# Kernel tuning notes

Measured on AMD Instinct MI355X. Metric: run time of the kernel, lower is better.

Reference implementation:

```python
import jax, jax.numpy as jnp
import numpy as np

B, T, C = 2, 2048, 1024
H = 16
D = C // H  # head_dim = 64
SCALE = D ** -0.5


def setup_inputs() -> dict:
    key = jax.random.key(0)
    ks = jax.random.split(key, 5)
    x = jax.random.normal(ks[0], (B, T, C), dtype=jnp.float32)
    # causal mask: -inf above diagonal, 0 elsewhere (module checks mask == -inf)
    neg_inf = jnp.float32(-jnp.inf)
    causal = jnp.where(jnp.tril(jnp.ones((T, T), dtype=bool)), 0.0, neg_inf)
    mask = causal[None, None, :, :].astype(jnp.float32)  # [1,1,T,T]
    # xavier_normal for [C, C] linear weights: std = sqrt(2/(C+C))
    std = float(np.sqrt(2.0 / (C + C)))
    wq = jax.random.normal(ks[1], (C, C), dtype=jnp.float32) * std
    wk = jax.random.normal(ks[2], (C, C), dtype=jnp.float32) * std
    wv = jax.random.normal(ks[3], (C, C), dtype=jnp.float32) * std
    wo = jax.random.normal(ks[4], (C, C), dtype=jnp.float32) * std
    return {"x": x, "mask": mask, "wq": wq, "wk": wk, "wv": wv, "wo": wo}


def reference(x, mask, wq, wk, wv, wo):
    # torch nn.Linear: y = x @ W.T
    q = jnp.einsum('btc,oc->bto', x, wq).reshape(B, T, H, D).transpose(0, 2, 1, 3)
    k = jnp.einsum('btc,oc->bto', x, wk).reshape(B, T, H, D).transpose(0, 2, 1, 3)
    v = jnp.einsum('btc,oc->bto', x, wv).reshape(B, T, H, D).transpose(0, 2, 1, 3)
    scores = jnp.einsum('bhqd,bhkd->bhqk', q, k) * SCALE  # [B,H,T,T]
    scores = jnp.where(mask == -jnp.inf, -jnp.inf, scores)
    attn = jax.nn.softmax(scores, axis=-1)
    out = jnp.einsum('bhqk,bhkd->bhqd', attn, v)  # [B,H,T,D]
    out = out.transpose(0, 2, 1, 3).reshape(B, T, C)
    return jnp.einsum('btc,oc->bto', out, wo)
```

## Files before the change

### kernel.cpp

```cpp
#include <hip/hip_runtime.h>
#include <hip/hip_bf16.h>


typedef __bf16 bf16_t;
typedef __bf16 bf16x8 __attribute__((ext_vector_type(8)));
typedef __bf16 bf16x4 __attribute__((ext_vector_type(4)));
typedef __bf16 bf16x2 __attribute__((ext_vector_type(2)));
typedef float  f32x4  __attribute__((ext_vector_type(4)));
typedef unsigned u32x4 __attribute__((ext_vector_type(4)));

__device__ __forceinline__ void gload_lds16(const bf16_t* g, bf16_t* l) {
  __builtin_amdgcn_global_load_lds((__attribute__((address_space(1))) void*)g,
                                   (__attribute__((address_space(3))) void*)l, 16, 0, 0);
}

__device__ __forceinline__ unsigned pack_bf16(float a, float b) {
  bf16x2 v; v[0] = (bf16_t)a; v[1] = (bf16_t)b;
  return __builtin_bit_cast(unsigned, v);
}

__global__ __launch_bounds__(256) void cvt_f32_bf16(const float* __restrict__ in,
                                                    bf16_t* __restrict__ out, int n4) {
  int i = blockIdx.x * 256 + threadIdx.x;
  if (i >= n4) return;
  float4 v = reinterpret_cast<const float4*>(in)[i];
  bf16x4 o;
  o[0] = (bf16_t)v.x; o[1] = (bf16_t)v.y; o[2] = (bf16_t)v.z; o[3] = (bf16_t)v.w;
  reinterpret_cast<bf16x4*>(out)[i] = o;
}

__global__ __launch_bounds__(256) void cvt_w4(const float* __restrict__ i0, const float* __restrict__ i1,
                                              const float* __restrict__ i2, const float* __restrict__ i3,
                                              bf16_t* __restrict__ o0, bf16_t* __restrict__ o1,
                                              bf16_t* __restrict__ o2, bf16_t* __restrict__ o3) {
  int which = blockIdx.y;
  const float* in = (which == 0) ? i0 : (which == 1) ? i1 : (which == 2) ? i2 : i3;
  bf16_t* out     = (which == 0) ? o0 : (which == 1) ? o1 : (which == 2) ? o2 : o3;
  int i = blockIdx.x * 256 + threadIdx.x;
  float4 v = reinterpret_cast<const float4*>(in)[i];
  bf16x4 o;
  o[0] = (bf16_t)v.x; o[1] = (bf16_t)v.y; o[2] = (bf16_t)v.z; o[3] = (bf16_t)v.w;
  reinterpret_cast<bf16x4*>(out)[i] = o;
}

#define TM 128
#define TN 128
#define TK 64

__global__ __launch_bounds__(256) void gemm_bt(
    const bf16_t* __restrict__ A,
    const bf16_t* __restrict__ W0, const bf16_t* __restrict__ W1, const bf16_t* __restrict__ W2,
    bf16_t* __restrict__ O0, bf16_t* __restrict__ O1, bf16_t* __restrict__ O2,
    float* __restrict__ OF, int kind)
{
  __shared__ alignas(16) bf16_t As[TM * TK];
  __shared__ alignas(16) bf16_t Bs[TN * TK];
  const int K = 1024;
  const int t = threadIdx.x;
  const int lane = t & 63;
  const int w = t >> 6;
  const int wr = w >> 1, wc = w & 1;
  const int lo = lane & 15, hi = lane >> 4;
  const int m0 = blockIdx.x * TM, n0 = blockIdx.y * TN;

  int mode;
  const bf16_t* Bw;
  bf16_t* outb = nullptr;
  if (kind == 1) { mode = 3; Bw = W0; }
  else {
    mode = blockIdx.z;
    Bw   = (mode == 0) ? W0 : (mode == 1) ? W1 : W2;
    outb = (mode == 0) ? O0 : (mode == 1) ? O1 : O2;
  }

  f32x4 acc[4][4] = {};
  const int srow = t >> 3;
  const int sch  = t & 7;

  for (int k0 = 0; k0 < K; k0 += TK) {
#pragma unroll
    for (int r = 0; r < 4; ++r) {
      int row = r * 32 + srow;
      gload_lds16(A  + (size_t)(m0 + row) * K + k0 + sch * 8, &As[row * TK + sch * 8]);
      gload_lds16(Bw + (size_t)(n0 + row) * K + k0 + sch * 8, &Bs[row * TK + sch * 8]);
    }
    __syncthreads();
#pragma unroll
    for (int ks = 0; ks < 2; ++ks) {
      bf16x8 af[4], bfr[4];
#pragma unroll
      for (int i = 0; i < 4; ++i) {
        af[i]  = *reinterpret_cast<const bf16x8*>(&As[(wr * 64 + i * 16 + lo) * TK + ks * 32 + hi * 8]);
        bfr[i] = *reinterpret_cast<const bf16x8*>(&Bs[(wc * 64 + i * 16 + lo) * TK + ks * 32 + hi * 8]);
      }
#pragma unroll
      for (int i = 0; i < 4; ++i)
#pragma unroll
        for (int j = 0; j < 4; ++j)
          acc[i][j] = __builtin_amdgcn_mfma_f32_16x16x32_bf16(af[i], bfr[j], acc[i][j], 0, 0, 0);
    }
    __syncthreads();
  }

#pragma unroll
  for (int i = 0; i < 4; ++i)
#pragma unroll
    for (int j = 0; j < 4; ++j)
#pragma unroll
      for (int r = 0; r < 4; ++r) {
        int m = m0 + wr * 64 + i * 16 + hi * 4 + r;
        int n = n0 + wc * 64 + j * 16 + lo;
        float v = acc[i][j][r];
        if (mode == 3) {
          OF[(size_t)m * 1024 + n] = v;
        } else {
          int b = m >> 11, tq = m & 2047;
          int h = n >> 6,  d  = n & 63;
          if (mode == 0) v *= 0.18033688011f;
          size_t addr = (mode == 2)
              ? ((size_t)(b * 16 + h) * 64 + d) * 2048 + tq
              : ((size_t)(b * 16 + h) * 2048 + tq) * 64 + d;
          outb[addr] = (bf16_t)v;
        }
      }
}

#define SLAB 8832

__global__ __launch_bounds__(256) void attn_fwd(
    const bf16_t* __restrict__ Q,
    const bf16_t* __restrict__ Km,
    const bf16_t* __restrict__ Vt,
    bf16_t* __restrict__ att)
{
  __shared__ alignas(16) char smem[4 * SLAB];
  const int t = threadIdx.x, lane = t & 63, w = t >> 6;
  const int lo = lane & 15, h = lane >> 4;
  const int item = blockIdx.x;
  const int bh = item >> 5;
  const int pr = item & 31;
  const bf16_t* Qb = Q  + (size_t)bh * 2048 * 64;
  const bf16_t* Kb = Km + (size_t)bh * 2048 * 64;
  const bf16_t* Vb = Vt + (size_t)bh * 64 * 2048;
  float* accW = (float*)(smem + w * SLAB);
  float* lW   = (float*)(smem + w * SLAB + 8704);
  const int b = bh >> 4, hd = bh & 15;
  const int src1 = lo + 32 * (h & 1);
  const int src2 = src1 + 16;
  const bool hsel = (h >> 1) != 0;

  auto run_tile = [&](int q0) {
    bf16x8 qf[2][2];
#pragma unroll
    for (int qt = 0; qt < 2; ++qt)
#pragma unroll
      for (int ks = 0; ks < 2; ++ks)
        qf[qt][ks] = *reinterpret_cast<const bf16x8*>(
            &Qb[(size_t)(q0 + qt * 16 + lo) * 64 + ks * 32 + h * 8]);

    f32x4 acc[2][4] = {};
    float lp[2] = {};
    const int kend = q0 + 32;
    for (int kb = w * 64; kb < kend; kb += 256) {
      f32x4 s_t[4][2] = {};
#pragma unroll
      for (int ks = 0; ks < 2; ++ks) {
        bf16x8 kf[4];
#pragma unroll
        for (int kt = 0; kt < 4; ++kt)
          kf[kt] = *reinterpret_cast<const bf16x8*>(
              &Kb[(size_t)(kb + kt * 16 + lo) * 64 + ks * 32 + h * 8]);
#pragma unroll
        for (int kt = 0; kt < 4; ++kt)
#pragma unroll
          for (int qt = 0; qt < 2; ++qt)
            s_t[kt][qt] = __builtin_amdgcn_mfma_f32_16x16x32_bf16(kf[kt], qf[qt][ks], s_t[kt][qt], 0, 0, 0);
      }
      bf16x8 vf[2][4];
#pragma unroll
      for (int kh = 0; kh < 2; ++kh)
#pragma unroll
        for (int dt = 0; dt < 4; ++dt)
          vf[kh][dt] = *reinterpret_cast<const bf16x8*>(
              &Vb[(size_t)(dt * 16 + lo) * 2048 + kb + kh * 32 + h * 8]);
      if (kb + 63 >= q0) {
#pragma unroll
        for (int kt = 0; kt < 4; ++kt)
#pragma unroll
          for (int qt = 0; qt < 2; ++qt)
#pragma unroll
            for (int r = 0; r < 4; ++r) {
              int kg = kb + kt * 16 + h * 4 + r;
              int qg = q0 + qt * 16 + lo;
              if (kg > qg) s_t[kt][qt][r] = -__builtin_inff();
            }
      }
      unsigned uP[2][4][2];
#pragma unroll
      for (int qt = 0; qt < 2; ++qt)
#pragma unroll
        for (int kt = 0; kt < 4; ++kt) {
          float p0 = exp2f(s_t[kt][qt][0]);
          float p1 = exp2f(s_t[kt][qt][1]);
          float p2 = exp2f(s_t[kt][qt][2]);
          float p3 = exp2f(s_t[kt][qt][3]);
          lp[qt] += (p0 + p1) + (p2 + p3);
          uP[qt][kt][0] = pack_bf16(p0, p1);
          uP[qt][kt][1] = pack_bf16(p2, p3);
        }
#pragma unroll
      for (int kh = 0; kh < 2; ++kh)
#pragma unroll
        for (int qt = 0; qt < 2; ++qt) {
          unsigned a0x = __shfl((int)uP[qt][2 * kh][0], src1);
          unsigned a0y = __shfl((int)uP[qt][2 * kh + 1][0], src1);
          unsigned a1x = __shfl((int)uP[qt][2 * kh][1], src1);
          unsigned a1y = __shfl((int)uP[qt][2 * kh + 1][1], src1);
          unsigned a2x = __shfl((int)uP[qt][2 * kh][0], src2);
          unsigned a2y = __shfl((int)uP[qt][2 * kh + 1][0], src2);
          unsigned a3x = __shfl((int)uP[qt][2 * kh][1], src2);
          unsigned a3y = __shfl((int)uP[qt][2 * kh + 1][1], src2);
          u32x4 au;
          au[0] = hsel ? a0y : a0x;
          au[1] = hsel ? a1y : a1x;
          au[2] = hsel ? a2y : a2x;
          au[3] = hsel ? a3y : a3x;
          bf16x8 pa = __builtin_bit_cast(bf16x8, au);
#pragma unroll
          for (int dt = 0; dt < 4; ++dt)
            acc[qt][dt] = __builtin_amdgcn_mfma_f32_16x16x32_bf16(pa, vf[kh][dt], acc[qt][dt], 0, 0, 0);
        }
    }

    float lrow[2];
#pragma unroll
    for (int qt = 0; qt < 2; ++qt) {
      float v = lp[qt];
      v += __shfl_xor(v, 16);
      v += __shfl_xor(v, 32);
      lrow[qt] = v;
    }

#pragma unroll
    for (int qt = 0; qt < 2; ++qt) {
#pragma unroll
      for (int r = 0; r < 4; ++r) {
        int row = qt * 16 + h * 4 + r;
#pragma unroll
        for (int dt = 0; dt < 4; ++dt)
          accW[row * 68 + dt * 16 + lo] = acc[qt][dt][r];
      }
      if (h == 0) lW[qt * 16 + lo] = lrow[qt];
    }
    __syncthreads();

    {
      const int row = t >> 3, c0 = (t & 7) * 8;
      float lsum = 0.f, o[8] = {};
#pragma unroll
      for (int w2 = 0; w2 < 4; ++w2) {
        lsum += ((const float*)(smem + w2 * SLAB + 8704))[row];
        const float* a2 = (const float*)(smem + w2 * SLAB) + row * 68 + c0;
#pragma unroll
        for (int j = 0; j < 8; ++j) o[j] += a2[j];
      }
      float inv = 1.f / lsum;
      bf16x8 ov;
#pragma unroll
      for (int j = 0; j < 8; ++j) ov[j] = (bf16_t)(o[j] * inv);
      *reinterpret_cast<bf16x8*>(&att[((size_t)(b * 2048 + q0 + row)) * 1024 + hd * 64 + c0]) = ov;
    }
    __syncthreads();
  };

  run_tile((63 - pr) * 32);
  run_tile(pr * 32);
}

extern "C" void kernel_launch(void* const* d_in, const int* in_sizes, int n_in,
                              void* d_out, int out_size, void* d_ws, size_t ws_size,
                              hipStream_t stream) {
  (void)in_sizes; (void)n_in; (void)out_size; (void)ws_size;
  const float* x  = (const float*)d_in[0];
  const float* wq = (const float*)d_in[2];
  const float* wk = (const float*)d_in[3];
  const float* wv = (const float*)d_in[4];
  const float* wo = (const float*)d_in[5];
  float* out = (float*)d_out;

  char* ws = (char*)d_ws;
  const size_t SZ_X = (size_t)4096 * 1024 * 2;
  const size_t SZ_W = (size_t)1024 * 1024 * 2;
  bf16_t* xb  = (bf16_t*)(ws);
  bf16_t* wqb = (bf16_t*)(ws + SZ_X);
  bf16_t* wkb = (bf16_t*)(ws + SZ_X + 1 * SZ_W);
  bf16_t* wvb = (bf16_t*)(ws + SZ_X + 2 * SZ_W);
  bf16_t* wob = (bf16_t*)(ws + SZ_X + 3 * SZ_W);
  bf16_t* qw  = (bf16_t*)(ws + 1 * SZ_X + 4 * SZ_W);
  bf16_t* kw  = (bf16_t*)(ws + 2 * SZ_X + 4 * SZ_W);
  bf16_t* vtw = (bf16_t*)(ws + 3 * SZ_X + 4 * SZ_W);
  bf16_t* att = xb;

  cvt_f32_bf16<<<4096, 256, 0, stream>>>(x, xb, 4096 * 1024 / 4);
  cvt_w4<<<dim3(1024, 4), 256, 0, stream>>>(wq, wk, wv, wo, wqb, wkb, wvb, wob);

  gemm_bt<<<dim3(32, 8, 3), 256, 0, stream>>>(xb, wqb, wkb, wvb, qw, kw, vtw, nullptr, 0);
  attn_fwd<<<1024, 256, 0, stream>>>(qw, kw, vtw, att);
  gemm_bt<<<dim3(32, 8, 1), 256, 0, stream>>>(att, wob, nullptr, nullptr,
                                              nullptr, nullptr, nullptr, out, 1);
}
```

Before: 169.2 us.

## Double-buffer GEMM LDS tiles, remap attention blocks, raise MFMA wave priority

The projection GEMM now uses two LDS buffers per operand and prefetches the next K tile with async global-to-LDS loads while computing on the current one, waiting with vmcnt and a raw s_barrier. The attention kernel remaps block indices so consecutive blocks spread across heads and query tiles, which may change L2 locality and load balance. It also wraps MFMA groups in s_setprio to favour waves issuing matrix instructions. Double buffering doubles GEMM LDS use, which can lower occupancy, and the hand-written vmcnt count must match the number of outstanding loads.

```diff
diff --git a/kernel.cpp b/kernel.cpp
--- a/kernel.cpp
+++ b/kernel.cpp
@@ -53,9 +53,9 @@
     bf16_t* __restrict__ O0, bf16_t* __restrict__ O1, bf16_t* __restrict__ O2,
     float* __restrict__ OF, int kind)
 {
-  __shared__ alignas(16) bf16_t As[TM * TK];
-  __shared__ alignas(16) bf16_t Bs[TN * TK];
-  const int K = 1024;
+  __shared__ alignas(16) bf16_t As[2][TM * TK];
+  __shared__ alignas(16) bf16_t Bs[2][TN * TK];
+  const int K = 1024, NT = K / TK;
   const int t = threadIdx.x;
   const int lane = t & 63;
   const int w = t >> 6;
@@ -77,21 +77,32 @@
   const int srow = t >> 3;
   const int sch  = t & 7;
 
-  for (int k0 = 0; k0 < K; k0 += TK) {
+  auto stage = [&](int buf, int k0) {
 #pragma unroll
     for (int r = 0; r < 4; ++r) {
       int row = r * 32 + srow;
-      gload_lds16(A  + (size_t)(m0 + row) * K + k0 + sch * 8, &As[row * TK + sch * 8]);
-      gload_lds16(Bw + (size_t)(n0 + row) * K + k0 + sch * 8, &Bs[row * TK + sch * 8]);
-    }
-    __syncthreads();
+      gload_lds16(A  + (size_t)(m0 + row) * K + k0 + sch * 8, &As[buf][row * TK + sch * 8]);
+      gload_lds16(Bw + (size_t)(n0 + row) * K + k0 + sch * 8, &Bs[buf][row * TK + sch * 8]);
+    }
+  };
+
+  stage(0, 0);
+  for (int ti = 0; ti < NT; ++ti) {
+    const int cur = ti & 1;
+    if (ti + 1 < NT) {
+      stage(cur ^ 1, (ti + 1) * TK);
+      asm volatile("s_waitcnt vmcnt(8)" ::: "memory");
+    } else {
+      asm volatile("s_waitcnt vmcnt(0)" ::: "memory");
+    }
+    __builtin_amdgcn_s_barrier();
 #pragma unroll
     for (int ks = 0; ks < 2; ++ks) {
       bf16x8 af[4], bfr[4];
 #pragma unroll
       for (int i = 0; i < 4; ++i) {
-        af[i]  = *reinterpret_cast<const bf16x8*>(&As[(wr * 64 + i * 16 + lo) * TK + ks * 32 + hi * 8]);
-        bfr[i] = *reinterpret_cast<const bf16x8*>(&Bs[(wc * 64 + i * 16 + lo) * TK + ks * 32 + hi * 8]);
+        af[i]  = *reinterpret_cast<const bf16x8*>(&As[cur][(wr * 64 + i * 16 + lo) * TK + ks * 32 + hi * 8]);
+        bfr[i] = *reinterpret_cast<const bf16x8*>(&Bs[cur][(wc * 64 + i * 16 + lo) * TK + ks * 32 + hi * 8]);
       }
 #pragma unroll
       for (int i = 0; i < 4; ++i)
@@ -99,7 +110,7 @@
         for (int j = 0; j < 4; ++j)
           acc[i][j] = __builtin_amdgcn_mfma_f32_16x16x32_bf16(af[i], bfr[j], acc[i][j], 0, 0, 0);
     }
-    __syncthreads();
+    __builtin_amdgcn_s_barrier();
   }
 
 #pragma unroll
@@ -136,7 +147,8 @@
   __shared__ alignas(16) char smem[4 * SLAB];
   const int t = threadIdx.x, lane = t & 63, w = t >> 6;
   const int lo = lane & 15, h = lane >> 4;
-  const int item = blockIdx.x;
+  const int blk = blockIdx.x;
+  const int item = (blk & 7) * 128 + (blk >> 3);
   const int bh = item >> 5;
   const int pr = item & 31;
   const bf16_t* Qb = Q  + (size_t)bh * 2048 * 64;
@@ -170,11 +182,13 @@
         for (int kt = 0; kt < 4; ++kt)
           kf[kt] = *reinterpret_cast<const bf16x8*>(
               &Kb[(size_t)(kb + kt * 16 + lo) * 64 + ks * 32 + h * 8]);
+        __builtin_amdgcn_s_setprio(1);
 #pragma unroll
         for (int kt = 0; kt < 4; ++kt)
 #pragma unroll
           for (int qt = 0; qt < 2; ++qt)
             s_t[kt][qt] = __builtin_amdgcn_mfma_f32_16x16x32_bf16(kf[kt], qf[qt][ks], s_t[kt][qt], 0, 0, 0);
+        __builtin_amdgcn_s_setprio(0);
       }
       bf16x8 vf[2][4];
 #pragma unroll
@@ -226,9 +240,11 @@
           au[2] = hsel ? a2y : a2x;
           au[3] = hsel ? a3y : a3x;
           bf16x8 pa = __builtin_bit_cast(bf16x8, au);
+          __builtin_amdgcn_s_setprio(1);
 #pragma unroll
           for (int dt = 0; dt < 4; ++dt)
             acc[qt][dt] = __builtin_amdgcn_mfma_f32_16x16x32_bf16(pa, vf[kh][dt], acc[qt][dt], 0, 0, 0);
+          __builtin_amdgcn_s_setprio(0);
         }
     }
 
```

Result: slower. 173.0 us (+2.3%).

## Merge conversion kernels, vectorize V-transpose stores, swizzle attention blocks, raise MFMA priority

Applied to the files above, without the earlier changes.

The two f32-to-bf16 conversion kernels become one launch, which saves a kernel launch. The V-projection epilogue now packs four consecutive tq values into one bf16x4 store instead of four scalar strided stores. The attention block index is remapped so that consecutive blocks are spread across different (b,h) groups, probably to balance causal work across XCDs or to improve cache locality. s_setprio calls are placed around the MFMA sections. Each of these is a small independent change, and the remapping could affect L2 reuse.

```diff
diff --git a/kernel.cpp b/kernel.cpp
--- a/kernel.cpp
+++ b/kernel.cpp
@@ -19,24 +19,21 @@
   return __builtin_bit_cast(unsigned, v);
 }
 
-__global__ __launch_bounds__(256) void cvt_f32_bf16(const float* __restrict__ in,
-                                                    bf16_t* __restrict__ out, int n4) {
-  int i = blockIdx.x * 256 + threadIdx.x;
-  if (i >= n4) return;
-  float4 v = reinterpret_cast<const float4*>(in)[i];
-  bf16x4 o;
-  o[0] = (bf16_t)v.x; o[1] = (bf16_t)v.y; o[2] = (bf16_t)v.z; o[3] = (bf16_t)v.w;
-  reinterpret_cast<bf16x4*>(out)[i] = o;
-}
-
-__global__ __launch_bounds__(256) void cvt_w4(const float* __restrict__ i0, const float* __restrict__ i1,
-                                              const float* __restrict__ i2, const float* __restrict__ i3,
-                                              bf16_t* __restrict__ o0, bf16_t* __restrict__ o1,
-                                              bf16_t* __restrict__ o2, bf16_t* __restrict__ o3) {
-  int which = blockIdx.y;
-  const float* in = (which == 0) ? i0 : (which == 1) ? i1 : (which == 2) ? i2 : i3;
-  bf16_t* out     = (which == 0) ? o0 : (which == 1) ? o1 : (which == 2) ? o2 : o3;
-  int i = blockIdx.x * 256 + threadIdx.x;
+__global__ __launch_bounds__(256) void cvt_all(
+    const float* __restrict__ x,  const float* __restrict__ i0, const float* __restrict__ i1,
+    const float* __restrict__ i2, const float* __restrict__ i3,
+    bf16_t* __restrict__ ox, bf16_t* __restrict__ o0, bf16_t* __restrict__ o1,
+    bf16_t* __restrict__ o2, bf16_t* __restrict__ o3) {
+  int blk = blockIdx.x;
+  const float* in; bf16_t* out; int i;
+  if (blk < 4096) { in = x; out = ox; i = blk * 256 + threadIdx.x; }
+  else {
+    int wb = blk - 4096;
+    int which = wb >> 10;
+    in  = (which == 0) ? i0 : (which == 1) ? i1 : (which == 2) ? i2 : i3;
+    out = (which == 0) ? o0 : (which == 1) ? o1 : (which == 2) ? o2 : o3;
+    i = (wb & 1023) * 256 + threadIdx.x;
+  }
   float4 v = reinterpret_cast<const float4*>(in)[i];
   bf16x4 o;
   o[0] = (bf16_t)v.x; o[1] = (bf16_t)v.y; o[2] = (bf16_t)v.z; o[3] = (bf16_t)v.w;
@@ -102,27 +99,41 @@
     __syncthreads();
   }
 
-#pragma unroll
-  for (int i = 0; i < 4; ++i)
-#pragma unroll
-    for (int j = 0; j < 4; ++j)
-#pragma unroll
-      for (int r = 0; r < 4; ++r) {
-        int m = m0 + wr * 64 + i * 16 + hi * 4 + r;
+  if (mode == 2) {
+#pragma unroll
+    for (int i = 0; i < 4; ++i)
+#pragma unroll
+      for (int j = 0; j < 4; ++j) {
+        int m = m0 + wr * 64 + i * 16 + hi * 4;
         int n = n0 + wc * 64 + j * 16 + lo;
-        float v = acc[i][j][r];
-        if (mode == 3) {
-          OF[(size_t)m * 1024 + n] = v;
-        } else {
-          int b = m >> 11, tq = m & 2047;
-          int h = n >> 6,  d  = n & 63;
-          if (mode == 0) v *= 0.18033688011f;
-          size_t addr = (mode == 2)
-              ? ((size_t)(b * 16 + h) * 64 + d) * 2048 + tq
-              : ((size_t)(b * 16 + h) * 2048 + tq) * 64 + d;
-          outb[addr] = (bf16_t)v;
+        int b = m >> 11, tq = m & 2047;
+        int h = (n >> 6) & 15, d = n & 63;
+        bf16x4 pk;
+#pragma unroll
+        for (int r = 0; r < 4; ++r) pk[r] = (bf16_t)acc[i][j][r];
+        *reinterpret_cast<bf16x4*>(
+            &outb[((size_t)(b * 16 + h) * 64 + d) * 2048 + tq]) = pk;
+      }
+  } else {
+#pragma unroll
+    for (int i = 0; i < 4; ++i)
+#pragma unroll
+      for (int j = 0; j < 4; ++j)
+#pragma unroll
+        for (int r = 0; r < 4; ++r) {
+          int m = m0 + wr * 64 + i * 16 + hi * 4 + r;
+          int n = n0 + wc * 64 + j * 16 + lo;
+          float v = acc[i][j][r];
+          if (mode == 3) {
+            OF[(size_t)m * 1024 + n] = v;
+          } else {
+            int b = m >> 11, tq = m & 2047;
+            int h = n >> 6,  d  = n & 63;
+            if (mode == 0) v *= 0.18033688011f;
+            outb[((size_t)(b * 16 + h) * 2048 + tq) * 64 + d] = (bf16_t)v;
+          }
         }
-      }
+  }
 }
 
 #define SLAB 8832
@@ -136,7 +147,8 @@
   __shared__ alignas(16) char smem[4 * SLAB];
   const int t = threadIdx.x, lane = t & 63, w = t >> 6;
   const int lo = lane & 15, h = lane >> 4;
-  const int item = blockIdx.x;
+  const int blk = blockIdx.x;
+  const int item = (blk & 7) * 128 + (blk >> 3);
   const int bh = item >> 5;
   const int pr = item & 31;
   const bf16_t* Qb = Q  + (size_t)bh * 2048 * 64;
@@ -170,11 +182,13 @@
         for (int kt = 0; kt < 4; ++kt)
           kf[kt] = *reinterpret_cast<const bf16x8*>(
               &Kb[(size_t)(kb + kt * 16 + lo) * 64 + ks * 32 + h * 8]);
+        __builtin_amdgcn_s_setprio(1);
 #pragma unroll
         for (int kt = 0; kt < 4; ++kt)
 #pragma unroll
           for (int qt = 0; qt < 2; ++qt)
             s_t[kt][qt] = __builtin_amdgcn_mfma_f32_16x16x32_bf16(kf[kt], qf[qt][ks], s_t[kt][qt], 0, 0, 0);
+        __builtin_amdgcn_s_setprio(0);
       }
       bf16x8 vf[2][4];
 #pragma unroll
@@ -226,9 +240,11 @@
           au[2] = hsel ? a2y : a2x;
           au[3] = hsel ? a3y : a3x;
           bf16x8 pa = __builtin_bit_cast(bf16x8, au);
+          __builtin_amdgcn_s_setprio(1);
 #pragma unroll
           for (int dt = 0; dt < 4; ++dt)
             acc[qt][dt] = __builtin_amdgcn_mfma_f32_16x16x32_bf16(pa, vf[kh][dt], acc[qt][dt], 0, 0, 0);
+          __builtin_amdgcn_s_setprio(0);
         }
     }
 
@@ -301,8 +317,7 @@
   bf16_t* vtw = (bf16_t*)(ws + 3 * SZ_X + 4 * SZ_W);
   bf16_t* att = xb;
 
-  cvt_f32_bf16<<<4096, 256, 0, stream>>>(x, xb, 4096 * 1024 / 4);
-  cvt_w4<<<dim3(1024, 4), 256, 0, stream>>>(wq, wk, wv, wo, wqb, wkb, wvb, wob);
+  cvt_all<<<8192, 256, 0, stream>>>(x, wq, wk, wv, wo, xb, wqb, wkb, wvb, wob);
 
   gemm_bt<<<dim3(32, 8, 3), 256, 0, stream>>>(xb, wqb, wkb, wvb, qw, kw, vtw, nullptr, 0);
   attn_fwd<<<1024, 256, 0, stream>>>(qw, kw, vtw, att);
```

Result: faster. 155.6 us (-8.0%).
